# Kernel tuning notes

Hardware: AMD Instinct MI355X
Metric: run time of the kernel (lower is better)

The kernel has to match this reference:

```python
import jax, jax.numpy as jnp
import numpy as np
from jax import lax

EPS = 1e-5      # BatchNorm1d default eps
SLOPE = 0.01    # LeakyReLU default negative_slope
DN = ('NCDHW', 'OIDHW', 'NCDHW')
PAD_31 = ((1, 1), (0, 0), (1, 1))   # kernel (3,1,3), padding (1,0,1)
PAD_13 = ((0, 0), (1, 1), (1, 1))   # kernel (1,3,3), padding (0,1,1)
PAD_P = ((1, 1), (1, 1), (1, 1))    # pool kernel 3, padding 1
STRIDE_P = (2, 2, 1)                # height_pooling=False -> stride (2,2,1)


def setup_inputs() -> dict:
    key = jax.random.key(0)
    ks = jax.random.split(key, 8)
    B, Cin, Cout = 1, 32, 64
    D1, D2, D3 = 160, 160, 32
    mask = jax.random.randint(ks[0], (B, 1, D1, D2, D3), 0, 2) > 0
    x = jax.random.normal(ks[1], (B, Cin, D1, D2, D3), dtype=jnp.float32)

    def w(k, cin, cout, kd, kh, kw):
        return jax.random.normal(k, (cout, cin, kd, kh, kw), dtype=jnp.float32) * 0.05

    inp = {
        'x': x, 'mask': mask,
        'W_A1': w(ks[2], Cin, Cout, 3, 1, 3),
        'W_A2': w(ks[3], Cout, Cout, 1, 3, 3),
        'W_B1': w(ks[4], Cin, Cout, 1, 3, 3),
        'W_B2': w(ks[5], Cout, Cout, 3, 1, 3),
        'W_pool': w(ks[6], Cout, Cout, 3, 3, 3),
    }
    for name in ('A1', 'A2', 'B1', 'B2'):
        inp['g_' + name] = jnp.ones((Cout,), jnp.float32)
        inp['b_' + name] = jnp.zeros((Cout,), jnp.float32)
    return inp


def _conv(h, W, pad, stride=(1, 1, 1)):
    return lax.conv_general_dilated(h, W, stride, pad, dimension_numbers=DN)


def _lrelu(h):
    return jnp.where(h >= 0, h, SLOPE * h)


def _masked_bn(h, m, n_active, gamma, beta):
    # BatchNorm1d over the [N_active, C] sparse feature tensor:
    # per-channel stats over active voxels only (biased variance, training mode).
    mean = jnp.sum(h * m, axis=(0, 2, 3, 4)) / n_active
    mu = mean[None, :, None, None, None]
    var = jnp.sum(((h - mu) ** 2) * m, axis=(0, 2, 3, 4)) / n_active
    inv = lax.rsqrt(var + EPS)[None, :, None, None, None]
    out = (h - mu) * inv * gamma[None, :, None, None, None] + beta[None, :, None, None, None]
    return out * m  # keep inactive sites exactly zero


def reference(x, mask, W_A1, W_A2, W_B1, W_B2, W_pool,
              g_A1, b_A1, g_A2, b_A2, g_B1, b_B1, g_B2, b_B2):
    m = mask.astype(x.dtype)                      # [B,1,D1,D2,D3] active-site indicator
    n_active = jnp.sum(m)
    xs = x * m                                    # sparse input: zero at inactive voxels

    def subm(h, W, pad):
        # submanifold conv: compute only at active output sites (same site set as input)
        return _conv(h, W, pad) * m

    # branch A: conv3x1 -> LeakyReLU -> BN -> conv1x3 -> LeakyReLU -> BN
    res_A = _masked_bn(_lrelu(subm(xs, W_A1, PAD_31)), m, n_active, g_A1, b_A1)
    res_A = _masked_bn(_lrelu(subm(res_A, W_A2, PAD_13)), m, n_active, g_A2, b_A2)

    # branch B: conv1x3 -> LeakyReLU -> BN -> conv3x1 -> LeakyReLU -> BN
    res_B = _masked_bn(_lrelu(subm(xs, W_B1, PAD_13)), m, n_active, g_B1, b_B1)
    res_B = _masked_bn(_lrelu(subm(res_B, W_B2, PAD_31)), m, n_active, g_B2, b_B2)

    res_B = res_B + res_A

    # strided SparseConv3d pool: output active where any input in 3x3x3 window is active
    ones_k = jnp.ones((1, 1, 3, 3, 3), x.dtype)
    out_mask = (_conv(m, ones_k, PAD_P, STRIDE_P) > 0).astype(x.dtype)
    down = _conv(res_B, W_pool, PAD_P, STRIDE_P) * out_mask
    return (down, res_B)
```

## Files before the change

kernel.cpp:

```cpp
#include <hip/hip_runtime.h>

static constexpr int ND1=160, ND2=160, ND3=32;
static constexpr int SP  = ND1*ND2*ND3;
static constexpr int CO  = 64;
static constexpr int OD1=80, OD2=80, OD3=32;
static constexpr int OSP = OD1*OD2*OD3;
static constexpr int NSC = 64;

typedef __attribute__((ext_vector_type(8))) short  short8;
typedef __attribute__((ext_vector_type(4))) float  f32x4;

__device__ __forceinline__ float b2f(unsigned u){ return __uint_as_float(u<<16); }
__device__ __forceinline__ unsigned short f2b(float f){
    unsigned u = __float_as_uint(f);
    u += 0x7fffu + ((u>>16)&1u);
    return (unsigned short)(u>>16);
}

__global__ void k_detect(const unsigned char* __restrict__ mb, int* __restrict__ flag)
{
    __shared__ int lf;
    if (threadIdx.x == 0) lf = 0;
    __syncthreads();
    int f = 0;
    for (int i = blockIdx.x*256 + threadIdx.x; i < SP; i += gridDim.x*256) {
        unsigned char b = mb[i];
        if (b > 1) f |= 4;
        if (b != 0 && (i & 3)) f |= 1;
    }
    if (f) atomicOr(&lf, f);
    __syncthreads();
    if (threadIdx.x == 0 && lf) atomicOr(flag, lf);
}

__global__ void k_mask(const void* __restrict__ mraw, const int* __restrict__ flag,
                       float* __restrict__ m, float* __restrict__ nactN)
{
    int i = blockIdx.x*256 + threadIdx.x;
    int f = *flag;
    float v;
    if (f & 4)      v = (reinterpret_cast<const float*>(mraw)[i] != 0.f) ? 1.f : 0.f;
    else if (f & 1) v = (reinterpret_cast<const unsigned char*>(mraw)[i] != 0) ? 1.f : 0.f;
    else            v = (reinterpret_cast<const int*>(mraw)[i] != 0) ? 1.f : 0.f;
    m[i] = v;
    float s = v;
    #pragma unroll
    for (int off = 32; off > 0; off >>= 1) s += __shfl_xor(s, off);
    __shared__ float wsum[4];
    if ((threadIdx.x & 63) == 0) wsum[threadIdx.x >> 6] = s;
    __syncthreads();
    if (threadIdx.x == 0) atomicAdd(&nactN[blockIdx.x & (NSC-1)], wsum[0]+wsum[1]+wsum[2]+wsum[3]);
}

__global__ void k_outmask(const float* __restrict__ m, float* __restrict__ om)
{
    int i = blockIdx.x*256 + threadIdx.x;
    int o3 = i & 31; int t = i >> 5; int o2 = t % OD2; int o1 = t / OD2;
    float s = 0.f;
    for (int kd = 0; kd < 3; kd++) { int d1 = 2*o1 - 1 + kd; if ((unsigned)d1 >= ND1) continue;
      for (int kh = 0; kh < 3; kh++) { int d2 = 2*o2 - 1 + kh; if ((unsigned)d2 >= ND2) continue;
        for (int kw = 0; kw < 3; kw++) { int d3 = o3 - 1 + kw; if ((unsigned)d3 >= ND3) continue;
          s += m[(d1*ND2 + d2)*ND3 + d3];
        } } }
    om[i] = (s > 0.f) ? 1.f : 0.f;
}

__global__ void k_finalize2(const float* __restrict__ SN0, const float* __restrict__ g0,
                            const float* __restrict__ b0, float* __restrict__ o0,
                            const float* __restrict__ SN1, const float* __restrict__ g1,
                            const float* __restrict__ b1, float* __restrict__ o1,
                            const float* __restrict__ nactN)
{
    const float* SN = blockIdx.x ? SN1 : SN0;
    const float* g  = blockIdx.x ? g1  : g0;
    const float* b  = blockIdx.x ? b1  : b0;
    float*       o  = blockIdx.x ? o1  : o0;
    int c = threadIdx.x;
    float s1 = 0.f, s2 = 0.f;
    #pragma unroll 4
    for (int k = 0; k < NSC; k++){
        s1 += SN[k*128 + c];
        s2 += SN[k*128 + 64 + c];
    }
    float nn = nactN[c];
    #pragma unroll
    for (int off = 32; off > 0; off >>= 1) nn += __shfl_xor(nn, off);
    float mean = s1 / nn;
    float var  = s2 / nn - mean*mean;
    float inv  = rsqrtf(var + 1e-5f);
    float sc   = inv * g[c];
    o[c]      = sc;
    o[64 + c] = b[c] - mean*sc;
}

__global__ void k_wprep(const float* __restrict__ W, unsigned short* __restrict__ Wt,
                        int CIN, int NT)
{
    int i = blockIdx.x*256 + threadIdx.x;
    int K = CIN*NT;
    if (i >= 64*K) return;
    int ksub = i & 31;
    int t = i >> 5;
    int co = t & 63;
    int kc = t >> 6;
    int nch = CIN >> 5;
    int tap = kc / nch;
    int ci  = (kc - tap*nch)*32 + ksub;
    Wt[i] = f2b(W[((size_t)co*CIN + ci)*NT + tap]);
}

__global__ void k_prep_x(const float* __restrict__ x, const float* __restrict__ m,
                         unsigned short* __restrict__ xt)
{
    __shared__ float t[64][33];
    int sp0 = blockIdx.x*64;
    int tid = threadIdx.x;
    int c = tid>>6, s = tid&63;
    float mm = m[sp0+s];
    #pragma unroll
    for (int r=0;r<8;r++){
        int ci = c + r*4;
        t[s][ci] = x[(size_t)ci*SP + sp0 + s]*mm;
    }
    __syncthreads();
    int sp = tid>>2, c0 = (tid&3)*8;
    unsigned short o[8];
    #pragma unroll
    for (int i=0;i<8;i++) o[i] = f2b(t[sp][c0+i]);
    uint4 pk;
    pk.x = o[0] | ((unsigned)o[1]<<16);
    pk.y = o[2] | ((unsigned)o[3]<<16);
    pk.z = o[4] | ((unsigned)o[5]<<16);
    pk.w = o[6] | ((unsigned)o[7]<<16);
    *reinterpret_cast<uint4*>(xt + (size_t)(sp0+sp)*32 + c0) = pk;
}

__global__ void k_resB(const unsigned short* __restrict__ hA, const unsigned short* __restrict__ hB,
                       const float* __restrict__ sA, const float* __restrict__ sB,
                       const float* __restrict__ m,
                       unsigned short* __restrict__ rbt, float* __restrict__ resf)
{
    __shared__ float t[64][65];
    __shared__ float ss[256];
    int tid = threadIdx.x;
    if (tid < 128){ ss[tid] = sA[tid]; ss[128+tid] = sB[tid]; }
    __syncthreads();
    int sp0 = blockIdx.x*64;
    int sp = tid>>2, c0 = (tid&3)*16;
    float mm = m[sp0+sp];
    const size_t base = (size_t)(sp0+sp)*64 + c0;
    uint4 a0 = *reinterpret_cast<const uint4*>(hA + base);
    uint4 a1 = *reinterpret_cast<const uint4*>(hA + base + 8);
    uint4 b0 = *reinterpret_cast<const uint4*>(hB + base);
    uint4 b1 = *reinterpret_cast<const uint4*>(hB + base + 8);
    unsigned ua[16] = {a0.x&0xffffu,a0.x>>16,a0.y&0xffffu,a0.y>>16,a0.z&0xffffu,a0.z>>16,a0.w&0xffffu,a0.w>>16,
                       a1.x&0xffffu,a1.x>>16,a1.y&0xffffu,a1.y>>16,a1.z&0xffffu,a1.z>>16,a1.w&0xffffu,a1.w>>16};
    unsigned ub[16] = {b0.x&0xffffu,b0.x>>16,b0.y&0xffffu,b0.y>>16,b0.z&0xffffu,b0.z>>16,b0.w&0xffffu,b0.w>>16,
                       b1.x&0xffffu,b1.x>>16,b1.y&0xffffu,b1.y>>16,b1.z&0xffffu,b1.z>>16,b1.w&0xffffu,b1.w>>16};
    unsigned short o[16];
    #pragma unroll
    for (int q=0;q<16;q++){
        int ci = c0+q;
        float v = (b2f(ua[q])*ss[ci] + ss[64+ci] + b2f(ub[q])*ss[128+ci] + ss[192+ci])*mm;
        t[sp][ci] = v;
        o[q] = f2b(v);
    }
    uint4 p0, p1;
    p0.x = o[0]|((unsigned)o[1]<<16);  p0.y = o[2]|((unsigned)o[3]<<16);
    p0.z = o[4]|((unsigned)o[5]<<16);  p0.w = o[6]|((unsigned)o[7]<<16);
    p1.x = o[8]|((unsigned)o[9]<<16);  p1.y = o[10]|((unsigned)o[11]<<16);
    p1.z = o[12]|((unsigned)o[13]<<16); p1.w = o[14]|((unsigned)o[15]<<16);
    *reinterpret_cast<uint4*>(rbt + base)     = p0;
    *reinterpret_cast<uint4*>(rbt + base + 8) = p1;
    __syncthreads();
    int ci = tid>>2, s0 = (tid&3)*16;
    #pragma unroll
    for (int kq=0;kq<4;kq++){
        float4 ov;
        ov.x = t[s0+4*kq+0][ci]; ov.y = t[s0+4*kq+1][ci];
        ov.z = t[s0+4*kq+2][ci]; ov.w = t[s0+4*kq+3][ci];
        *reinterpret_cast<float4*>(resf + (size_t)ci*SP + sp0 + s0 + 4*kq) = ov;
    }
}

template<int KIND, int CIN, bool HASAFF>
__launch_bounds__(256, (CIN==32) ? 3 : 2)
__global__ void mconv10(const unsigned short* __restrict__ in,
                        const unsigned short* __restrict__ Wt,
                        const float* __restrict__ scsh,
                        const float* __restrict__ mstage,
                        const float* __restrict__ mout,
                        unsigned short* __restrict__ outb,
                        float* __restrict__ statsN)
{
    constexpr int NCH  = CIN/32;
    constexpr int NKC  = NCH*9;
    constexpr int NR   = 10;
    constexpr int ROWB = 34*CIN*2;
    constexpr int SWZ  = (CIN==64) ? 7 : 3;
    __shared__ __align__(16) char lds[NR*ROWB];
    __shared__ float sst[128];

    const int tid = threadIdx.x;
    const int w = tid>>6, l = tid&63, g = l>>4, lj = l&15;
    const int h = w&1, rg = w>>1;

    int gi = (blockIdx.x & 7)*(gridDim.x>>3) + (blockIdx.x>>3);
    int z  = gi % 160;
    int r0 = (gi / 160)*8;

    if (tid < 128) sst[tid] = 0.f;

    const int sd3 = tid>>3;
    const int k0  = (tid&7)*(CIN/8);

    float sc[8], sh[8];
    if (HASAFF){
        #pragma unroll
        for (int j=0;j<8;j++){ sc[j]=scsh[k0+j]; sh[j]=scsh[64+k0+j]; }
    }

    for (int i = tid; i < NR*2*(CIN/8); i += 256){
        int per = CIN/8;
        int rr = i / (2*per);
        int rem = i - rr*2*per;
        int slot = (rem >= per) ? 33 : 0;
        int kc16 = (rem >= per) ? (rem - per) : rem;
        int dst = rr*ROWB + slot*CIN*2 + kc16*16;
        dst ^= ((slot&SWZ)<<4);
        *reinterpret_cast<uint4*>(lds + dst) = make_uint4(0,0,0,0);
    }

    if (CIN==64){
        uint4 v[NR]; float mmr[NR];
        #pragma unroll
        for (int rr=0; rr<NR; rr++){
            int rw = r0 - 1 + rr;
            v[rr] = make_uint4(0,0,0,0); mmr[rr] = 0.f;
            if ((unsigned)rw < 160u){
                int vox = (KIND==0) ? ((rw*ND2 + z)*ND3 + sd3)
                                    : ((z*ND2 + rw)*ND3 + sd3);
                v[rr] = *reinterpret_cast<const uint4*>(in + (size_t)vox*CIN + k0);
                if (HASAFF) mmr[rr] = mstage[vox];
            }
        }
        #pragma unroll
        for (int rr=0; rr<NR; rr++){
            uint4 vv = v[rr];
            if (HASAFF){
                float mm = mmr[rr];
                unsigned us[8] = {vv.x&0xffffu,vv.x>>16,vv.y&0xffffu,vv.y>>16,
                                  vv.z&0xffffu,vv.z>>16,vv.w&0xffffu,vv.w>>16};
                unsigned short o[8];
                #pragma unroll
                for (int j=0;j<8;j++) o[j] = f2b((b2f(us[j])*sc[j]+sh[j])*mm);
                vv.x = o[0]|((unsigned)o[1]<<16); vv.y = o[2]|((unsigned)o[3]<<16);
                vv.z = o[4]|((unsigned)o[5]<<16); vv.w = o[6]|((unsigned)o[7]<<16);
            }
            int dst = (rr*ROWB + (((sd3+1)*CIN + k0)*2)) ^ (((sd3+1)&SWZ)<<4);
            *reinterpret_cast<uint4*>(lds + dst) = vv;
        }
    } else {
        uint2 v[NR];
        #pragma unroll
        for (int rr=0; rr<NR; rr++){
            int rw = r0 - 1 + rr;
            v[rr] = make_uint2(0,0);
            if ((unsigned)rw < 160u){
                int vox = (KIND==0) ? ((rw*ND2 + z)*ND3 + sd3)
                                    : ((z*ND2 + rw)*ND3 + sd3);
                v[rr] = *reinterpret_cast<const uint2*>(in + (size_t)vox*CIN + k0);
            }
        }
        #pragma unroll
        for (int rr=0; rr<NR; rr++){
            int dst = (rr*ROWB + (((sd3+1)*CIN + k0)*2)) ^ (((sd3+1)&SWZ)<<4);
            *reinterpret_cast<uint2*>(lds + dst) = v[rr];
        }
    }

    short8 pa[NKC][2];
    {
        const unsigned short* wb = Wt + (size_t)(h*32)*32 + lj*32 + g*8;
        #pragma unroll
        for (int kc=0; kc<NKC; kc++){
            pa[kc][0] = *reinterpret_cast<const short8*>(wb + (size_t)kc*2048);
            pa[kc][1] = *reinterpret_cast<const short8*>(wb + (size_t)kc*2048 + 512);
        }
    }

    int tb[8], ovox[8];
    float mm[8];
    #pragma unroll
    for (int t=0;t<8;t++){
        int rowb = rg*4 + (t>>1);
        int o3   = (t&1)*16 + lj;
        tb[t] = rowb*ROWB + ((o3*CIN + g*8)*2);
        int o2r = r0 + rowb;
        ovox[t] = (KIND==0) ? ((o2r*ND2 + z)*ND3 + o3)
                            : ((z*ND2 + o2r)*ND3 + o3);
        mm[t] = mout[ovox[t]];
    }
    int swz[3];
    #pragma unroll
    for (int kw=0;kw<3;kw++) swz[kw] = ((lj+kw)&SWZ)<<4;

    __syncthreads();

    f32x4 acc[2][8];
    #pragma unroll
    for (int c=0;c<2;c++)
        #pragma unroll
        for (int t=0;t<8;t++)
            #pragma unroll
            for (int q=0;q<4;q++) acc[c][t][q] = 0.f;

    #pragma unroll
    for (int ch=0; ch<NCH; ch++){
        #pragma unroll
        for (int tap=0; tap<9; tap++){
            const int kd = tap/3, kw = tap - kd*3;
            const int kc = tap*NCH + ch;
            const int tapoff = kd*ROWB + (kw*CIN + ch*32)*2;
            #pragma unroll
            for (int t=0;t<8;t++){
                int off = (tb[t] + tapoff) ^ swz[kw];
                short8 bv = *reinterpret_cast<const short8*>(lds + off);
                acc[0][t] = __builtin_amdgcn_mfma_f32_16x16x32_bf16(pa[kc][0], bv, acc[0][t], 0,0,0);
                acc[1][t] = __builtin_amdgcn_mfma_f32_16x16x32_bf16(pa[kc][1], bv, acc[1][t], 0,0,0);
            }
        }
    }

    #pragma unroll
    for (int c=0;c<2;c++){
        const int ct = h*2 + c;
        float s1[4] = {0.f,0.f,0.f,0.f};
        float s2[4] = {0.f,0.f,0.f,0.f};
        #pragma unroll
        for (int t=0;t<8;t++){
            float v[4];
            #pragma unroll
            for (int r=0;r<4;r++){
                float xv = acc[c][t][r]*mm[t];
                xv = (xv >= 0.f) ? xv : 0.01f*xv;
                v[r] = xv; s1[r] += xv; s2[r] += xv*xv;
            }
            unsigned lo = f2b(v[0]) | ((unsigned)f2b(v[1])<<16);
            unsigned hi = f2b(v[2]) | ((unsigned)f2b(v[3])<<16);
            *reinterpret_cast<uint2*>(outb + (size_t)ovox[t]*64 + ct*16 + g*4) = make_uint2(lo,hi);
        }
        #pragma unroll
        for (int r=0;r<4;r++){
            float a = s1[r], b = s2[r];
            a += __shfl_xor(a,1); b += __shfl_xor(b,1);
            a += __shfl_xor(a,2); b += __shfl_xor(b,2);
            a += __shfl_xor(a,4); b += __shfl_xor(b,4);
            a += __shfl_xor(a,8); b += __shfl_xor(b,8);
            if (lj == 0){
                atomicAdd(&sst[ct*16 + g*4 + r], a);
                atomicAdd(&sst[64 + ct*16 + g*4 + r], b);
            }
        }
    }
    __syncthreads();
    if (tid < 128){
        float* sg = statsN + (size_t)(blockIdx.x & (NSC-1))*128;
        atomicAdd(&sg[tid], sst[tid]);
    }
}

__launch_bounds__(256, 2)
__global__ void mpool4(const unsigned short* __restrict__ in,
                       const unsigned short* __restrict__ Wt,
                       const float* __restrict__ mout,
                       float* __restrict__ outf)
{
    constexpr int SLOTB = 80;
    constexpr int ROWB  = 34*SLOTB;
    extern __shared__ __align__(16) char lds[];

    const int tid = threadIdx.x;
    const int w = tid>>6, l = tid&63, g = l>>4, lj = l&15;
    const int h = w&1, rg = w>>1;

    int gi = (blockIdx.x & 7)*(gridDim.x>>3) + (blockIdx.x>>3);
    int z  = gi % OD1;
    int r0 = (gi / OD1)*4;

    const int sd3 = tid>>3;
    const int kq  = tid&7;

    for (int i = tid; i < 27*2*4; i += 256){
        int row = i >> 3, rem = i & 7;
        int slot = (rem >= 4) ? 33 : 0;
        int c16 = rem & 3;
        *reinterpret_cast<uint4*>(lds + row*ROWB + slot*SLOTB + c16*16) = make_uint4(0,0,0,0);
    }

    int ovx[4];
    float om[4];
    #pragma unroll
    for (int t=0;t<4;t++){
        int row = rg*2 + (t>>1);
        int o3  = (t&1)*16 + lj;
        ovx[t] = (z*OD2 + (r0 + row))*OD3 + o3;
        om[t]  = mout[ovx[t]];
    }

    f32x4 acc[2][4];
    #pragma unroll
    for (int c=0;c<2;c++)
        #pragma unroll
        for (int t=0;t<4;t++)
            #pragma unroll
            for (int q=0;q<4;q++) acc[c][t][q] = 0.f;

    const unsigned short* wbase = Wt + (size_t)(h*32)*32 + lj*32 + g*8;

    #pragma unroll 1
    for (int ph=0; ph<2; ph++){
        uint2 v[27];
        #pragma unroll
        for (int i=0;i<27;i++){
            const int kd = i/9, rr = i - (i/9)*9;
            int d1 = 2*z - 1 + kd;
            int d2 = 2*r0 - 1 + rr;
            v[i] = make_uint2(0,0);
            if ((unsigned)d1 < (unsigned)ND1 && (unsigned)d2 < (unsigned)ND2){
                int vox = (d1*ND2 + d2)*ND3 + sd3;
                v[i] = *reinterpret_cast<const uint2*>(in + (size_t)vox*64 + ph*32 + kq*4);
            }
        }
        __syncthreads();
        #pragma unroll
        for (int i=0;i<27;i++){
            *reinterpret_cast<uint2*>(lds + i*ROWB + (sd3+1)*SLOTB + kq*8) = v[i];
        }
        __syncthreads();

        #pragma unroll
        for (int kd=0; kd<3; kd++){
            short8 pa[9][2];
            #pragma unroll
            for (int tap=0; tap<9; tap++){
                const int kc = (kd*9 + tap)*2 + ph;
                pa[tap][0] = *reinterpret_cast<const short8*>(wbase + (size_t)kc*2048);
                pa[tap][1] = *reinterpret_cast<const short8*>(wbase + (size_t)kc*2048 + 512);
            }
            #pragma unroll
            for (int tap=0; tap<9; tap++){
                const int kh = tap/3, kw = tap - (tap/3)*3;
                #pragma unroll
                for (int t=0;t<4;t++){
                    const int rr = 2*(rg*2 + (t>>1)) + kh;
                    const int slot = (t&1)*16 + lj + kw;
                    const char* bp = lds + (kd*9 + rr)*ROWB + slot*SLOTB + g*16;
                    short8 bv = *reinterpret_cast<const short8*>(bp);
                    acc[0][t] = __builtin_amdgcn_mfma_f32_16x16x32_bf16(pa[tap][0], bv, acc[0][t], 0,0,0);
                    acc[1][t] = __builtin_amdgcn_mfma_f32_16x16x32_bf16(pa[tap][1], bv, acc[1][t], 0,0,0);
                }
            }
        }
    }

    #pragma unroll
    for (int c=0;c<2;c++){
        const int ct = h*2 + c;
        #pragma unroll
        for (int t=0;t<4;t++){
            #pragma unroll
            for (int r=0;r<4;r++){
                int co = ct*16 + g*4 + r;
                outf[(size_t)co*OSP + ovx[t]] = acc[c][t][r]*om[t];
            }
        }
    }
}

extern "C" void kernel_launch(void* const* d_in, const int* in_sizes, int n_in,
                              void* d_out, int out_size, void* d_ws, size_t ws_size,
                              hipStream_t stream)
{
    const float* x      = (const float*)d_in[0];
    const void*  mraw   = d_in[1];
    const float* W_A1   = (const float*)d_in[2];
    const float* W_A2   = (const float*)d_in[3];
    const float* W_B1   = (const float*)d_in[4];
    const float* W_B2   = (const float*)d_in[5];
    const float* W_pool = (const float*)d_in[6];
    const float* g_A1 = (const float*)d_in[7],  *b_A1 = (const float*)d_in[8];
    const float* g_A2 = (const float*)d_in[9],  *b_A2 = (const float*)d_in[10];
    const float* g_B1 = (const float*)d_in[11], *b_B1 = (const float*)d_in[12];
    const float* g_B2 = (const float*)d_in[13], *b_B2 = (const float*)d_in[14];

    char* p = (char*)d_ws;
    float* m     = (float*)p; p += (size_t)SP*4;
    float* omask = (float*)p; p += (size_t)OSP*4;
    float* statsN= (float*)p; p += 4*NSC*128*4;
    float* scsh  = (float*)p; p += 4*128*4;
    float* nactN = (float*)p; p += NSC*4;
    int*   flag  = (int*)p;   p += 4;
    p += 252;
    unsigned short* WtA1 = (unsigned short*)p; p += 288*64*2;
    unsigned short* WtA2 = (unsigned short*)p; p += 576*64*2;
    unsigned short* WtB1 = (unsigned short*)p; p += 288*64*2;
    unsigned short* WtB2 = (unsigned short*)p; p += 576*64*2;
    unsigned short* WtP  = (unsigned short*)p; p += 1728*64*2;
    unsigned short* X = (unsigned short*)p; p += (size_t)SP*32*2;
    unsigned short* P = (unsigned short*)p; p += (size_t)SP*64*2;
    unsigned short* Q = (unsigned short*)p; p += (size_t)SP*64*2;
    unsigned short* R = (unsigned short*)p; p += (size_t)SP*64*2;

    float* down = (float*)d_out;
    float* resf = down + (size_t)CO*OSP;

    const int shmP = 27*34*80;
    hipFuncSetAttribute((const void*)&mpool4, hipFuncAttributeMaxDynamicSharedMemorySize, shmP);

    hipMemsetAsync(statsN, 0, (4*NSC*128 + 4*128 + NSC)*4 + 4, stream);
    k_detect<<<256, 256, 0, stream>>>((const unsigned char*)mraw, flag);
    k_mask<<<SP/256, 256, 0, stream>>>(mraw, flag, m, nactN);
    k_outmask<<<OSP/256, 256, 0, stream>>>(m, omask);
    k_prep_x<<<SP/64, 256, 0, stream>>>(x, m, X);

    k_wprep<<<(64*288+255)/256, 256, 0, stream>>>(W_A1, WtA1, 32, 9);
    k_wprep<<<(64*576+255)/256, 256, 0, stream>>>(W_A2, WtA2, 64, 9);
    k_wprep<<<(64*288+255)/256, 256, 0, stream>>>(W_B1, WtB1, 32, 9);
    k_wprep<<<(64*576+255)/256, 256, 0, stream>>>(W_B2, WtB2, 64, 9);
    k_wprep<<<(64*1728+255)/256, 256, 0, stream>>>(W_pool, WtP, 64, 27);

    float* SA1 = statsN + 0*NSC*128;
    float* SA2 = statsN + 1*NSC*128;
    float* SB1 = statsN + 2*NSC*128;
    float* SB2 = statsN + 3*NSC*128;

    mconv10<0,32,false><<<3200, 256, 0, stream>>>(X, WtA1, nullptr, nullptr, m, P, SA1);
    mconv10<1,32,false><<<3200, 256, 0, stream>>>(X, WtB1, nullptr, nullptr, m, Q, SB1);
    k_finalize2<<<2, 64, 0, stream>>>(SA1, g_A1, b_A1, scsh + 0,
                                      SB1, g_B1, b_B1, scsh + 256, nactN);
    mconv10<1,64,true><<<3200, 256, 0, stream>>>(P, WtA2, scsh + 0,   m, m, R, SA2);
    mconv10<0,64,true><<<3200, 256, 0, stream>>>(Q, WtB2, scsh + 256, m, m, P, SB2);
    k_finalize2<<<2, 64, 0, stream>>>(SA2, g_A2, b_A2, scsh + 128,
                                      SB2, g_B2, b_B2, scsh + 384, nactN);
    k_resB<<<SP/64, 256, 0, stream>>>(R, P, scsh + 128, scsh + 384, m, Q, resf);
    mpool4<<<1600, 256, shmP, stream>>>(Q, WtP, omask, down);
}
```

Measured before the change: 667.8 us.

## Merge paired branch convs into dual launches and stage pool output through LDS

The branch-A and branch-B convolutions at each stage now run in a single 6400-block launch, with the kind (axis orientation) chosen at runtime per block half. A separate S buffer is added so the second stage no longer writes into P. The five weight-prep kernels become one, and the output-mask computation moves into k_prep_x, which cuts launch count and tail gaps. The pool kernel now writes its results to LDS first and then stores them as coalesced 16-byte vectors instead of scattered scalar stores, at the cost of an extra barrier and more workspace.

```diff
diff --git a/kernel.cpp b/kernel.cpp
--- a/kernel.cpp
+++ b/kernel.cpp
@@ -50,19 +50,6 @@
     if ((threadIdx.x & 63) == 0) wsum[threadIdx.x >> 6] = s;
     __syncthreads();
     if (threadIdx.x == 0) atomicAdd(&nactN[blockIdx.x & (NSC-1)], wsum[0]+wsum[1]+wsum[2]+wsum[3]);
-}
-
-__global__ void k_outmask(const float* __restrict__ m, float* __restrict__ om)
-{
-    int i = blockIdx.x*256 + threadIdx.x;
-    int o3 = i & 31; int t = i >> 5; int o2 = t % OD2; int o1 = t / OD2;
-    float s = 0.f;
-    for (int kd = 0; kd < 3; kd++) { int d1 = 2*o1 - 1 + kd; if ((unsigned)d1 >= ND1) continue;
-      for (int kh = 0; kh < 3; kh++) { int d2 = 2*o2 - 1 + kh; if ((unsigned)d2 >= ND2) continue;
-        for (int kw = 0; kw < 3; kw++) { int d3 = o3 - 1 + kw; if ((unsigned)d3 >= ND3) continue;
-          s += m[(d1*ND2 + d2)*ND3 + d3];
-        } } }
-    om[i] = (s > 0.f) ? 1.f : 0.f;
 }
 
 __global__ void k_finalize2(const float* __restrict__ SN0, const float* __restrict__ g0,
@@ -93,24 +80,34 @@
     o[64 + c] = b[c] - mean*sc;
 }
 
-__global__ void k_wprep(const float* __restrict__ W, unsigned short* __restrict__ Wt,
-                        int CIN, int NT)
+__global__ void k_wprep_all(const float* __restrict__ WA1, const float* __restrict__ WA2,
+                            const float* __restrict__ WB1, const float* __restrict__ WB2,
+                            const float* __restrict__ WP,
+                            unsigned short* __restrict__ tA1, unsigned short* __restrict__ tA2,
+                            unsigned short* __restrict__ tB1, unsigned short* __restrict__ tB2,
+                            unsigned short* __restrict__ tP)
 {
     int i = blockIdx.x*256 + threadIdx.x;
-    int K = CIN*NT;
-    if (i >= 64*K) return;
-    int ksub = i & 31;
-    int t = i >> 5;
+    const float* W; unsigned short* Wt; int CIN, NT, base;
+    if      (i < 18432)  { W=WA1; Wt=tA1; CIN=32; NT=9;  base=0; }
+    else if (i < 55296)  { W=WA2; Wt=tA2; CIN=64; NT=9;  base=18432; }
+    else if (i < 73728)  { W=WB1; Wt=tB1; CIN=32; NT=9;  base=55296; }
+    else if (i < 110592) { W=WB2; Wt=tB2; CIN=64; NT=9;  base=73728; }
+    else if (i < 221184) { W=WP;  Wt=tP;  CIN=64; NT=27; base=110592; }
+    else return;
+    int j = i - base;
+    int ksub = j & 31;
+    int t = j >> 5;
     int co = t & 63;
     int kc = t >> 6;
     int nch = CIN >> 5;
     int tap = kc / nch;
     int ci  = (kc - tap*nch)*32 + ksub;
-    Wt[i] = f2b(W[((size_t)co*CIN + ci)*NT + tap]);
+    Wt[j] = f2b(W[((size_t)co*CIN + ci)*NT + tap]);
 }
 
 __global__ void k_prep_x(const float* __restrict__ x, const float* __restrict__ m,
-                         unsigned short* __restrict__ xt)
+                         unsigned short* __restrict__ xt, float* __restrict__ om)
 {
     __shared__ float t[64][33];
     int sp0 = blockIdx.x*64;
@@ -133,6 +130,18 @@
     pk.z = o[4] | ((unsigned)o[5]<<16);
     pk.w = o[6] | ((unsigned)o[7]<<16);
     *reinterpret_cast<uint4*>(xt + (size_t)(sp0+sp)*32 + c0) = pk;
+
+    if (blockIdx.x < OSP/256){
+        int i = blockIdx.x*256 + tid;
+        int o3 = i & 31; int tt = i >> 5; int o2 = tt % OD2; int o1 = tt / OD2;
+        float ssum = 0.f;
+        for (int kd = 0; kd < 3; kd++) { int d1 = 2*o1 - 1 + kd; if ((unsigned)d1 >= ND1) continue;
+          for (int kh = 0; kh < 3; kh++) { int d2 = 2*o2 - 1 + kh; if ((unsigned)d2 >= ND2) continue;
+            for (int kw = 0; kw < 3; kw++) { int d3 = o3 - 1 + kw; if ((unsigned)d3 >= ND3) continue;
+              ssum += m[(d1*ND2 + d2)*ND3 + d3];
+            } } }
+        om[i] = (ssum > 0.f) ? 1.f : 0.f;
+    }
 }
 
 __global__ void k_resB(const unsigned short* __restrict__ hA, const unsigned short* __restrict__ hB,
@@ -183,15 +192,15 @@
     }
 }
 
-template<int KIND, int CIN, bool HASAFF>
+template<int CIN, bool HASAFF, int KA, int KB>
 __launch_bounds__(256, (CIN==32) ? 3 : 2)
-__global__ void mconv10(const unsigned short* __restrict__ in,
-                        const unsigned short* __restrict__ Wt,
-                        const float* __restrict__ scsh,
-                        const float* __restrict__ mstage,
-                        const float* __restrict__ mout,
-                        unsigned short* __restrict__ outb,
-                        float* __restrict__ statsN)
+__global__ void mconv_dual(const unsigned short* __restrict__ inA, const unsigned short* __restrict__ WtA,
+                           const float* __restrict__ scshA, unsigned short* __restrict__ outA,
+                           float* __restrict__ statsA,
+                           const unsigned short* __restrict__ inB, const unsigned short* __restrict__ WtB,
+                           const float* __restrict__ scshB, unsigned short* __restrict__ outB2,
+                           float* __restrict__ statsB,
+                           const float* __restrict__ mstage, const float* __restrict__ mout)
 {
     constexpr int NCH  = CIN/32;
     constexpr int NKC  = NCH*9;
@@ -205,7 +214,17 @@
     const int w = tid>>6, l = tid&63, g = l>>4, lj = l&15;
     const int h = w&1, rg = w>>1;
 
-    int gi = (blockIdx.x & 7)*(gridDim.x>>3) + (blockIdx.x>>3);
+    const int bid  = blockIdx.x;
+    const int hb   = (bid >= 3200) ? 1 : 0;
+    const int b2   = bid - hb*3200;
+    const int gi   = (b2&7)*400 + (b2>>3);
+    const int kind = hb ? KB : KA;
+    const unsigned short* in  = hb ? inB   : inA;
+    const unsigned short* Wt  = hb ? WtB   : WtA;
+    const float*        scsh  = hb ? scshB : scshA;
+    unsigned short*     outb  = hb ? outB2 : outA;
+    float*             statsN = hb ? statsB : statsA;
+
     int z  = gi % 160;
     int r0 = (gi / 160)*8;
 
@@ -238,7 +257,7 @@
             int rw = r0 - 1 + rr;
             v[rr] = make_uint4(0,0,0,0); mmr[rr] = 0.f;
             if ((unsigned)rw < 160u){
-                int vox = (KIND==0) ? ((rw*ND2 + z)*ND3 + sd3)
+                int vox = (kind==0) ? ((rw*ND2 + z)*ND3 + sd3)
                                     : ((z*ND2 + rw)*ND3 + sd3);
                 v[rr] = *reinterpret_cast<const uint4*>(in + (size_t)vox*CIN + k0);
                 if (HASAFF) mmr[rr] = mstage[vox];
@@ -267,7 +286,7 @@
             int rw = r0 - 1 + rr;
             v[rr] = make_uint2(0,0);
             if ((unsigned)rw < 160u){
-                int vox = (KIND==0) ? ((rw*ND2 + z)*ND3 + sd3)
+                int vox = (kind==0) ? ((rw*ND2 + z)*ND3 + sd3)
                                     : ((z*ND2 + rw)*ND3 + sd3);
                 v[rr] = *reinterpret_cast<const uint2*>(in + (size_t)vox*CIN + k0);
             }
@@ -297,7 +316,7 @@
         int o3   = (t&1)*16 + lj;
         tb[t] = rowb*ROWB + ((o3*CIN + g*8)*2);
         int o2r = r0 + rowb;
-        ovox[t] = (KIND==0) ? ((o2r*ND2 + z)*ND3 + o3)
+        ovox[t] = (kind==0) ? ((o2r*ND2 + z)*ND3 + o3)
                             : ((z*ND2 + o2r)*ND3 + o3);
         mm[t] = mout[ovox[t]];
     }
@@ -371,7 +390,7 @@
 }
 
 __launch_bounds__(256, 2)
-__global__ void mpool4(const unsigned short* __restrict__ in,
+__global__ void mpool5(const unsigned short* __restrict__ in,
                        const unsigned short* __restrict__ Wt,
                        const float* __restrict__ mout,
                        float* __restrict__ outf)
@@ -464,17 +483,31 @@
         }
     }
 
+    __syncthreads();
+    float* olds = (float*)lds;
     #pragma unroll
     for (int c=0;c<2;c++){
         const int ct = h*2 + c;
         #pragma unroll
         for (int t=0;t<4;t++){
+            int row = rg*2 + (t>>1);
+            int o3  = (t&1)*16 + lj;
             #pragma unroll
             for (int r=0;r<4;r++){
                 int co = ct*16 + g*4 + r;
-                outf[(size_t)co*OSP + ovx[t]] = acc[c][t][r]*om[t];
-            }
-        }
+                olds[co*128 + row*32 + o3] = acc[c][t][r]*om[t];
+            }
+        }
+    }
+    __syncthreads();
+    const size_t obase = (size_t)(z*OD2 + r0)*OD3;
+    #pragma unroll
+    for (int i=0;i<8;i++){
+        int idx = i*256 + tid;
+        int co  = idx >> 5;
+        int q   = idx & 31;
+        uint4 v = *reinterpret_cast<uint4*>(reinterpret_cast<char*>(olds) + co*512 + q*16);
+        *reinterpret_cast<uint4*>(outf + (size_t)co*OSP + obase + q*4) = v;
     }
 }
 
@@ -511,38 +544,36 @@
     unsigned short* P = (unsigned short*)p; p += (size_t)SP*64*2;
     unsigned short* Q = (unsigned short*)p; p += (size_t)SP*64*2;
     unsigned short* R = (unsigned short*)p; p += (size_t)SP*64*2;
+    unsigned short* S = (unsigned short*)p; p += (size_t)SP*64*2;
 
     float* down = (float*)d_out;
     float* resf = down + (size_t)CO*OSP;
 
     const int shmP = 27*34*80;
-    hipFuncSetAttribute((const void*)&mpool4, hipFuncAttributeMaxDynamicSharedMemorySize, shmP);
+    hipFuncSetAttribute((const void*)&mpool5, hipFuncAttributeMaxDynamicSharedMemorySize, shmP);
 
     hipMemsetAsync(statsN, 0, (4*NSC*128 + 4*128 + NSC)*4 + 4, stream);
     k_detect<<<256, 256, 0, stream>>>((const unsigned char*)mraw, flag);
     k_mask<<<SP/256, 256, 0, stream>>>(mraw, flag, m, nactN);
-    k_outmask<<<OSP/256, 256, 0, stream>>>(m, omask);
-    k_prep_x<<<SP/64, 256, 0, stream>>>(x, m, X);
-
-    k_wprep<<<(64*288+255)/256, 256, 0, stream>>>(W_A1, WtA1, 32, 9);
-    k_wprep<<<(64*576+255)/256, 256, 0, stream>>>(W_A2, WtA2, 64, 9);
-    k_wprep<<<(64*288+255)/256, 256, 0, stream>>>(W_B1, WtB1, 32, 9);
-    k_wprep<<<(64*576+255)/256, 256, 0, stream>>>(W_B2, WtB2, 64, 9);
-    k_wprep<<<(64*1728+255)/256, 256, 0, stream>>>(W_pool, WtP, 64, 27);
+    k_wprep_all<<<864, 256, 0, stream>>>(W_A1, W_A2, W_B1, W_B2, W_pool,
+                                         WtA1, WtA2, WtB1, WtB2, WtP);
+    k_prep_x<<<SP/64, 256, 0, stream>>>(x, m, X, omask);
 
     float* SA1 = statsN + 0*NSC*128;
     float* SA2 = statsN + 1*NSC*128;
     float* SB1 = statsN + 2*NSC*128;
     float* SB2 = statsN + 3*NSC*128;
 
-    mconv10<0,32,false><<<3200, 256, 0, stream>>>(X, WtA1, nullptr, nullptr, m, P, SA1);
-    mconv10<1,32,false><<<3200, 256, 0, stream>>>(X, WtB1, nullptr, nullptr, m, Q, SB1);
+    mconv_dual<32,false,0,1><<<6400, 256, 0, stream>>>(
+        X, WtA1, nullptr, P, SA1,
+        X, WtB1, nullptr, Q, SB1, nullptr, m);
     k_finalize2<<<2, 64, 0, stream>>>(SA1, g_A1, b_A1, scsh + 0,
                                       SB1, g_B1, b_B1, scsh + 256, nactN);
-    mconv10<1,64,true><<<3200, 256, 0, stream>>>(P, WtA2, scsh + 0,   m, m, R, SA2);
-    mconv10<0,64,true><<<3200, 256, 0, stream>>>(Q, WtB2, scsh + 256, m, m, P, SB2);
+    mconv_dual<64,true,1,0><<<6400, 256, 0, stream>>>(
+        P, WtA2, scsh + 0,   R, SA2,
+        Q, WtB2, scsh + 256, S, SB2, m, m);
     k_finalize2<<<2, 64, 0, stream>>>(SA2, g_A2, b_A2, scsh + 128,
                                       SB2, g_B2, b_B2, scsh + 384, nactN);
-    k_resB<<<SP/64, 256, 0, stream>>>(R, P, scsh + 128, scsh + 384, m, Q, resf);
-    mpool4<<<1600, 256, shmP, stream>>>(Q, WtP, omask, down);
-}
+    k_resB<<<SP/64, 256, 0, stream>>>(R, S, scsh + 128, scsh + 384, m, Q, resf);
+    mpool5<<<1600, 256, shmP, stream>>>(Q, WtP, omask, down);
+}
```

Result: faster. 638.7 us (-4.4%).
